# Optimization experiments

Measured on AMD Instinct MI355X. Metric: run time of the kernel, lower is better.

The kernel has to match this reference:

```python
import jax, jax.numpy as jnp
import numpy as np

B, N, K = 8, 2048, 20  # clouds, points per cloud, kNN neighbors
NUM_CLASSES = 40


def _mlp3(x, w1, b1, w2, b2, w3, b3):
    x = jax.nn.relu(x @ w1 + b1)
    x = jax.nn.relu(x @ w2 + b2)
    return jax.nn.relu(x @ w3 + b3)


def _dynamic_edge_conv(x, w1, b1, w2, b2, w3, b3):
    # x: [B, N, D]. Recompute kNN graph in feature space (per cloud),
    # build edge features [x_i, x_j - x_i], MLP, max-aggregate over neighbors.
    s = jnp.sum(x * x, axis=-1)  # [B, N]
    d2 = s[:, :, None] + s[:, None, :] - 2.0 * jnp.einsum('bnd,bmd->bnm', x, x)  # [B,N,N]
    _, idx = jax.lax.top_k(-d2, K)  # [B, N, K], includes self (dist 0), matching torch_cluster.knn(x, x)
    xj = jax.vmap(lambda xb, ib: xb[ib])(x, idx)  # gather neighbors [B, N, K, D]
    xi = jnp.broadcast_to(x[:, :, None, :], xj.shape)
    e = jnp.concatenate([xi, xj - xi], axis=-1)  # [B, N, K, 2D]
    h = _mlp3(e, w1, b1, w2, b2, w3, b3)  # [B, N, K, H]
    return jnp.max(h, axis=2)  # max aggregation -> [B, N, H]


def setup_inputs() -> dict:
    key = jax.random.key(0)
    ks = jax.random.split(key, 32)

    def w(k, shape):
        fan_in = shape[0]
        return (jax.random.normal(k, shape, dtype=jnp.float32) / np.sqrt(fan_in)).astype(jnp.float32)

    inp = {
        'pos': jax.random.normal(ks[0], (B * N, 3), dtype=jnp.float32),
        'batch': jnp.repeat(jnp.arange(B, dtype=jnp.int64), N),
        # conv1 MLP: 6 -> 64 -> 64 -> 64
        'c1w1': w(ks[1], (6, 64)),   'c1b1': jnp.zeros((64,), jnp.float32),
        'c1w2': w(ks[2], (64, 64)),  'c1b2': jnp.zeros((64,), jnp.float32),
        'c1w3': w(ks[3], (64, 64)),  'c1b3': jnp.zeros((64,), jnp.float32),
        # conv2 MLP: 128 -> 128 -> 128 -> 256
        'c2w1': w(ks[4], (128, 128)), 'c2b1': jnp.zeros((128,), jnp.float32),
        'c2w2': w(ks[5], (128, 128)), 'c2b2': jnp.zeros((128,), jnp.float32),
        'c2w3': w(ks[6], (128, 256)), 'c2b3': jnp.zeros((256,), jnp.float32),
        # classifier head
        'l0w': w(ks[7], (256, 512)),  'l0b': jnp.zeros((512,), jnp.float32),
        'l1w': w(ks[8], (512, 256)),  'l1b': jnp.zeros((256,), jnp.float32),
        'l2w': w(ks[9], (256, 256)),  'l2b': jnp.zeros((256,), jnp.float32),
        'l3w': w(ks[10], (256, NUM_CLASSES)), 'l3b': jnp.zeros((NUM_CLASSES,), jnp.float32),
    }
    return inp


def reference(pos, batch,
              c1w1, c1b1, c1w2, c1b2, c1w3, c1b3,
              c2w1, c2b1, c2w2, c2b2, c2w3, c2b3,
              l0w, l0b, l1w, l1b, l2w, l2b, l3w, l3b):
    # batch is a contiguous equal-size partition: reshape to [B, N, 3]
    x = pos.reshape(B, N, 3)
    x = _dynamic_edge_conv(x, c1w1, c1b1, c1w2, c1b2, c1w3, c1b3)   # [B, N, 64]
    x = _dynamic_edge_conv(x, c2w1, c2b1, c2w2, c2b2, c2w3, c2b3)   # [B, N, 256]
    x = jax.nn.relu(x @ l0w + l0b)                                   # [B, N, 512]
    x = jnp.max(x, axis=1)                                           # global_max_pool -> [B, 512]
    x = jax.nn.relu(x @ l1w + l1b)
    x = jax.nn.relu(x @ l2w + l2b)
    # dropout(p=0.5) is identity at inference
    x = x @ l3w + l3b
    return jax.nn.log_softmax(x, axis=-1)  # [B, NUM_CLASSES]
```

## Files before the change

### kernel.cpp

```cpp
#include <hip/hip_runtime.h>
#include <hip/hip_bf16.h>
#include <math.h>

#define BB 8
#define NN 2048
#define KK 20

typedef short bf16x8 __attribute__((ext_vector_type(8)));
typedef float f32x4 __attribute__((ext_vector_type(4)));

__device__ __forceinline__ unsigned short f2bf(float f) {
  unsigned u = __float_as_uint(f);
  u += 0x7FFFu + ((u >> 16) & 1u);
  return (unsigned short)(u >> 16);
}
__device__ __forceinline__ float bf2f(unsigned short h) {
  return __uint_as_float(((unsigned)h) << 16);
}

__device__ __forceinline__ void topk_insert(float d, int m, float (&bd)[KK], int (&bi)[KK],
                                            float& worst, int& wslot) {
  if (d < worst) {
#pragma unroll
    for (int j = 0; j < KK; ++j) {
      if (j == wslot) { bd[j] = d; bi[j] = m; }
    }
    float w = -INFINITY;
    int s = 0;
#pragma unroll
    for (int j = 0; j < KK; ++j) {
      if (bd[j] > w) { w = bd[j]; s = j; }
    }
    worst = w;
    wslot = s;
  }
}

__device__ __forceinline__ void sins20(float (&s)[KK], float d) {
#pragma unroll
  for (int q = 0; q < KK - 1; ++q) s[q] = fminf(s[q], fmaxf(s[q + 1], d));
  s[KK - 1] = fminf(s[KK - 1], d);
}

__device__ __forceinline__ float knn1_dist(float sn, float ssq,
                                           float x0, float x1, float x2,
                                           float y0, float y1, float y2) {
  const float dot = fmaf(x0, y0, fmaf(x1, y1, x2 * y2));
  return fmaf(-2.f, dot, sn + ssq);
}

__global__ __launch_bounds__(256) void knn1_part(const float* __restrict__ pos,
                                                 float* __restrict__ candd,
                                                 int* __restrict__ candi) {
  __shared__ float xs0[256], xs1[256], xs2[256], ss[256];
  const int bid = blockIdx.x;
  const int b = bid >> 6;
  const int nc = (bid >> 3) & 7;
  const int mc = bid & 7;
  const int t = threadIdx.x;
  const float* posb = pos + (size_t)b * NN * 3;
  {
    const int m = mc * 256 + t;
    const float a0 = posb[m * 3 + 0];
    const float a1 = posb[m * 3 + 1];
    const float a2 = posb[m * 3 + 2];
    xs0[t] = a0; xs1[t] = a1; xs2[t] = a2;
    ss[t] = a0 * a0 + a1 * a1 + a2 * a2;
  }
  __syncthreads();
  const int n = nc * 256 + t;
  const float xn0 = posb[n * 3 + 0];
  const float xn1 = posb[n * 3 + 1];
  const float xn2 = posb[n * 3 + 2];
  const float sn = xn0 * xn0 + xn1 * xn1 + xn2 * xn2;

  float s[KK];
#pragma unroll
  for (int q = 0; q < KK; ++q) s[q] = INFINITY;
  for (int lm = 0; lm < 256; lm += 8) {
    float dv[8];
#pragma unroll
    for (int u = 0; u < 8; ++u)
      dv[u] = knn1_dist(sn, ss[lm + u], xn0, xn1, xn2, xs0[lm + u], xs1[lm + u], xs2[lm + u]);
#pragma unroll
    for (int u = 0; u < 8; ++u) sins20(s, dv[u]);
  }
  const float tau = s[0];

  int cA = 0;
  for (int lm = 0; lm < 256; lm += 8) {
#pragma unroll
    for (int u = 0; u < 8; ++u) {
      const float d = knn1_dist(sn, ss[lm + u], xn0, xn1, xn2, xs0[lm + u], xs1[lm + u], xs2[lm + u]);
      cA += (d < tau) ? 1 : 0;
    }
  }

  int posA = 0, posB = cA;
  const int rbase = mc * 256;
  const size_t obase = ((size_t)(b * 8 + mc) * KK) * 2048 + n;
  for (int lm = 0; lm < 256; lm += 8) {
#pragma unroll
    for (int u = 0; u < 8; ++u) {
      const float d = knn1_dist(sn, ss[lm + u], xn0, xn1, xn2, xs0[lm + u], xs1[lm + u], xs2[lm + u]);
      if (d < tau) {
        candd[obase + (size_t)posA * 2048] = d;
        candi[obase + (size_t)posA * 2048] = rbase + lm + u;
        ++posA;
      } else if (d == tau && posB < KK) {
        candd[obase + (size_t)posB * 2048] = d;
        candi[obase + (size_t)posB * 2048] = rbase + lm + u;
        ++posB;
      }
    }
  }
}

template <int NCH, int G>
__global__ __launch_bounds__(256) void merge_topk2(const float* __restrict__ candd,
                                                   const int* __restrict__ candi,
                                                   int* __restrict__ idx_out) {
  const int gid = blockIdx.x * 256 + threadIdx.x;
  const int pt = gid / G;
  const int sub = gid % G;
  const int b = pt >> 11, n = pt & 2047;
  constexpr int CPT = NCH / G;
  float bd[KK]; int bi[KK];
#pragma unroll
  for (int j = 0; j < KK; ++j) { bd[j] = INFINITY; bi[j] = 0; }
  float worst = INFINITY;
  int wslot = 0;
#pragma unroll
  for (int cc = 0; cc < CPT; ++cc) {
    const int c = sub * CPT + cc;
    const size_t base = ((size_t)(b * NCH + c) * KK) * 2048 + n;
    float dv[KK]; int iv[KK];
#pragma unroll
    for (int j = 0; j < KK; ++j) dv[j] = candd[base + (size_t)j * 2048];
#pragma unroll
    for (int j = 0; j < KK; ++j) iv[j] = candi[base + (size_t)j * 2048];
#pragma unroll
    for (int j = 0; j < KK; ++j) topk_insert(dv[j], iv[j], bd, bi, worst, wslot);
  }
#pragma unroll
  for (int stride = 1; stride < G; stride <<= 1) {
    float od[KK]; int oi[KK];
#pragma unroll
    for (int q = 0; q < KK; ++q) {
      od[q] = __shfl_xor(bd[q], stride);
      oi[q] = __shfl_xor(bi[q], stride);
    }
#pragma unroll
    for (int q = 0; q < KK; ++q) topk_insert(od[q], oi[q], bd, bi, worst, wslot);
  }
  if (sub == 0) {
    int* op = idx_out + (size_t)pt * KK;
#pragma unroll
    for (int j = 0; j < KK; ++j) op[j] = bi[j];
  }
}

__global__ __launch_bounds__(256) void pre1_kernel(const float* __restrict__ pos,
                                                   const float* __restrict__ w1,
                                                   const float* __restrict__ b1,
                                                   float* __restrict__ U1,
                                                   float* __restrict__ V1) {
  const int t = threadIdx.x;
  const int c = t & 63;
  const int n = blockIdx.x * 4 + (t >> 6);
  const float p0 = pos[(size_t)n * 3 + 0];
  const float p1 = pos[(size_t)n * 3 + 1];
  const float p2 = pos[(size_t)n * 3 + 2];
  const float wt0 = w1[0 * 64 + c], wt1 = w1[1 * 64 + c], wt2 = w1[2 * 64 + c];
  const float wb0 = w1[3 * 64 + c], wb1 = w1[4 * 64 + c], wb2 = w1[5 * 64 + c];
  float v = p0 * wb0 + p1 * wb1 + p2 * wb2;
  float u = p0 * (wt0 - wb0) + p1 * (wt1 - wb1) + p2 * (wt2 - wb2) + b1[c];
  U1[(size_t)n * 64 + c] = u;
  V1[(size_t)n * 64 + c] = v;
}

__global__ __launch_bounds__(256) void pre2_kernel(const float* __restrict__ x1,
                                                   const float* __restrict__ w1,
                                                   const float* __restrict__ b1,
                                                   float* __restrict__ U,
                                                   float* __restrict__ V) {
  __shared__ float X[64][68];
  const int nbase = blockIdx.x * 64;
  const int t = threadIdx.x;
  for (int it = t; it < 1024; it += 256) {
    const int r = it >> 4, q = it & 15;
    *(float4*)&X[r][q * 4] = *(const float4*)&x1[(size_t)(nbase + r) * 64 + q * 4];
  }
  __syncthreads();
  const int ty = t >> 4, tx = t & 15;
  const int c0 = tx * 8;
  float accT[4][8], accB[4][8];
#pragma unroll
  for (int u = 0; u < 4; ++u)
#pragma unroll
    for (int i = 0; i < 8; ++i) { accT[u][i] = 0.f; accB[u][i] = 0.f; }
  for (int d0 = 0; d0 < 64; d0 += 4) {
    float4 a[4];
#pragma unroll
    for (int u = 0; u < 4; ++u) a[u] = *(const float4*)&X[ty * 4 + u][d0];
#pragma unroll
    for (int dd = 0; dd < 4; ++dd) {
      const float4 t0 = *(const float4*)&w1[(size_t)(d0 + dd) * 128 + c0];
      const float4 t1 = *(const float4*)&w1[(size_t)(d0 + dd) * 128 + c0 + 4];
      const float4 bb0 = *(const float4*)&w1[(size_t)(64 + d0 + dd) * 128 + c0];
      const float4 bb1 = *(const float4*)&w1[(size_t)(64 + d0 + dd) * 128 + c0 + 4];
#pragma unroll
      for (int u = 0; u < 4; ++u) {
        const float av = (dd == 0) ? a[u].x : (dd == 1) ? a[u].y : (dd == 2) ? a[u].z : a[u].w;
        accT[u][0] = fmaf(av, t0.x, accT[u][0]);
        accT[u][1] = fmaf(av, t0.y, accT[u][1]);
        accT[u][2] = fmaf(av, t0.z, accT[u][2]);
        accT[u][3] = fmaf(av, t0.w, accT[u][3]);
        accT[u][4] = fmaf(av, t1.x, accT[u][4]);
        accT[u][5] = fmaf(av, t1.y, accT[u][5]);
        accT[u][6] = fmaf(av, t1.z, accT[u][6]);
        accT[u][7] = fmaf(av, t1.w, accT[u][7]);
        accB[u][0] = fmaf(av, bb0.x, accB[u][0]);
        accB[u][1] = fmaf(av, bb0.y, accB[u][1]);
        accB[u][2] = fmaf(av, bb0.z, accB[u][2]);
        accB[u][3] = fmaf(av, bb0.w, accB[u][3]);
        accB[u][4] = fmaf(av, bb1.x, accB[u][4]);
        accB[u][5] = fmaf(av, bb1.y, accB[u][5]);
        accB[u][6] = fmaf(av, bb1.z, accB[u][6]);
        accB[u][7] = fmaf(av, bb1.w, accB[u][7]);
      }
    }
  }
  const float4 bA = *(const float4*)&b1[c0];
  const float4 bB = *(const float4*)&b1[c0 + 4];
#pragma unroll
  for (int u = 0; u < 4; ++u) {
    const size_t row = (size_t)(nbase + ty * 4 + u) * 128 + c0;
    float4 u0, u1, v0, v1;
    v0 = make_float4(accB[u][0], accB[u][1], accB[u][2], accB[u][3]);
    v1 = make_float4(accB[u][4], accB[u][5], accB[u][6], accB[u][7]);
    u0.x = accT[u][0] - accB[u][0] + bA.x;
    u0.y = accT[u][1] - accB[u][1] + bA.y;
    u0.z = accT[u][2] - accB[u][2] + bA.z;
    u0.w = accT[u][3] - accB[u][3] + bA.w;
    u1.x = accT[u][4] - accB[u][4] + bB.x;
    u1.y = accT[u][5] - accB[u][5] + bB.y;
    u1.z = accT[u][6] - accB[u][6] + bB.z;
    u1.w = accT[u][7] - accB[u][7] + bB.w;
    *(float4*)&U[row] = u0;
    *(float4*)&U[row + 4] = u1;
    *(float4*)&V[row] = v0;
    *(float4*)&V[row + 4] = v1;
  }
}

__global__ __launch_bounds__(256) void wprep_kernel(
    const float* __restrict__ c2w2, const float* __restrict__ c2w3,
    const float* __restrict__ c1w2, const float* __restrict__ c1w3,
    const float* __restrict__ l0w,
    unsigned short* __restrict__ w2t, unsigned short* __restrict__ w3t,
    unsigned short* __restrict__ c1w2hi, unsigned short* __restrict__ c1w2lo,
    unsigned short* __restrict__ c1w3hi, unsigned short* __restrict__ c1w3lo,
    unsigned short* __restrict__ l0thi, unsigned short* __restrict__ l0tlo) {
  const int i = blockIdx.x * 256 + threadIdx.x;
  if (i < 16384) {
    const int d = i >> 7, c = i & 127;
    w2t[c * 128 + d] = f2bf(c2w2[i]);
  } else if (i < 49152) {
    const int j = i - 16384;
    const int d = j >> 8, c = j & 255;
    w3t[c * 128 + d] = f2bf(c2w3[j]);
  } else if (i < 53248) {
    const int j = i - 49152;
    const int d = j >> 6, c = j & 63;
    const float v = c1w2[j];
    const unsigned short h = f2bf(v);
    c1w2hi[c * 64 + d] = h;
    c1w2lo[c * 64 + d] = f2bf(v - bf2f(h));
  } else if (i < 57344) {
    const int j = i - 53248;
    const int d = j >> 6, c = j & 63;
    const float v = c1w3[j];
    const unsigned short h = f2bf(v);
    c1w3hi[c * 64 + d] = h;
    c1w3lo[c * 64 + d] = f2bf(v - bf2f(h));
  } else if (i < 188416) {
    const int j = i - 57344;
    const int d = j >> 9, c = j & 511;
    const float v = l0w[j];
    const unsigned short h = f2bf(v);
    l0thi[c * 256 + d] = h;
    l0tlo[c * 256 + d] = f2bf(v - bf2f(h));
  }
}

__global__ __launch_bounds__(256) void conv1_kernel(
    const float* __restrict__ U1, const float* __restrict__ V1,
    const int* __restrict__ idx,
    const unsigned short* __restrict__ w2hi, const unsigned short* __restrict__ w2lo,
    const float* __restrict__ b2,
    const unsigned short* __restrict__ w3hi, const unsigned short* __restrict__ w3lo,
    const float* __restrict__ b3,
    float* __restrict__ xout) {
  __shared__ __align__(16) unsigned short A[160][2][76];
  __shared__ unsigned int pm[8][64];
  const int bid = blockIdx.x;
  const int b = bid >> 8;
  const int pbase = (bid & 255) * 8;
  const int t = threadIdx.x;
  const int wave = t >> 6, lane = t & 63;
  const int lrow = lane & 15;
  const int lk8 = (lane >> 4) * 8;
  const int c = wave * 16 + lrow;

  for (int it = t; it < 2560; it += 256) {
    const int r = it >> 4, q = it & 15;
    const int p = r / 20, k = r - (r / 20) * 20;
    const int n = b * NN + pbase + p;
    const int j = b * NN + idx[(size_t)n * KK + k];
    const float4 uv = *(const float4*)&U1[(size_t)n * 64 + q * 4];
    const float4 vv = *(const float4*)&V1[(size_t)j * 64 + q * 4];
    float e[4];
    e[0] = fmaxf(uv.x + vv.x, 0.f);
    e[1] = fmaxf(uv.y + vv.y, 0.f);
    e[2] = fmaxf(uv.z + vv.z, 0.f);
    e[3] = fmaxf(uv.w + vv.w, 0.f);
    ushort4 hi, lo;
    hi.x = f2bf(e[0]); lo.x = f2bf(e[0] - bf2f(hi.x));
    hi.y = f2bf(e[1]); lo.y = f2bf(e[1] - bf2f(hi.y));
    hi.z = f2bf(e[2]); lo.z = f2bf(e[2] - bf2f(hi.z));
    hi.w = f2bf(e[3]); lo.w = f2bf(e[3] - bf2f(hi.w));
    *(ushort4*)&A[r][0][q * 4] = hi;
    *(ushort4*)&A[r][1][q * 4] = lo;
  }
  for (int i = t; i < 512; i += 256) ((unsigned int*)pm)[i] = 0u;
  __syncthreads();

  {
    bf16x8 whi[2], wlo[2];
#pragma unroll
    for (int ks = 0; ks < 2; ++ks) {
      whi[ks] = *(const bf16x8*)&w2hi[(size_t)c * 64 + ks * 32 + lk8];
      wlo[ks] = *(const bf16x8*)&w2lo[(size_t)c * 64 + ks * 32 + lk8];
    }
    f32x4 acc2[10];
#pragma unroll
    for (int mt = 0; mt < 10; ++mt) {
      bf16x8 ahi[2], alo[2];
#pragma unroll
      for (int ks = 0; ks < 2; ++ks) {
        ahi[ks] = *(const bf16x8*)&A[mt * 16 + lrow][0][ks * 32 + lk8];
        alo[ks] = *(const bf16x8*)&A[mt * 16 + lrow][1][ks * 32 + lk8];
      }
      f32x4 acc = {0.f, 0.f, 0.f, 0.f};
#pragma unroll
      for (int ks = 0; ks < 2; ++ks) {
        acc = __builtin_amdgcn_mfma_f32_16x16x32_bf16(ahi[ks], whi[ks], acc, 0, 0, 0);
        acc = __builtin_amdgcn_mfma_f32_16x16x32_bf16(ahi[ks], wlo[ks], acc, 0, 0, 0);
        acc = __builtin_amdgcn_mfma_f32_16x16x32_bf16(alo[ks], whi[ks], acc, 0, 0, 0);
      }
      acc2[mt] = acc;
    }
    __syncthreads();
    const float bias = b2[c];
#pragma unroll
    for (int mt = 0; mt < 10; ++mt) {
      const int r0 = mt * 16 + ((lane >> 4) << 2);
#pragma unroll
      for (int reg = 0; reg < 4; ++reg) {
        const float v = fmaxf(acc2[mt][reg] + bias, 0.f);
        const unsigned short h = f2bf(v);
        A[r0 + reg][0][c] = h;
        A[r0 + reg][1][c] = f2bf(v - bf2f(h));
      }
    }
  }
  __syncthreads();

  {
    bf16x8 whi[2], wlo[2];
#pragma unroll
    for (int ks = 0; ks < 2; ++ks) {
      whi[ks] = *(const bf16x8*)&w3hi[(size_t)c * 64 + ks * 32 + lk8];
      wlo[ks] = *(const bf16x8*)&w3lo[(size_t)c * 64 + ks * 32 + lk8];
    }
    const float bias = b3[c];
#pragma unroll
    for (int mt = 0; mt < 10; ++mt) {
      bf16x8 ahi[2], alo[2];
#pragma unroll
      for (int ks = 0; ks < 2; ++ks) {
        ahi[ks] = *(const bf16x8*)&A[mt * 16 + lrow][0][ks * 32 + lk8];
        alo[ks] = *(const bf16x8*)&A[mt * 16 + lrow][1][ks * 32 + lk8];
      }
      f32x4 acc = {0.f, 0.f, 0.f, 0.f};
#pragma unroll
      for (int ks = 0; ks < 2; ++ks) {
        acc = __builtin_amdgcn_mfma_f32_16x16x32_bf16(ahi[ks], whi[ks], acc, 0, 0, 0);
        acc = __builtin_amdgcn_mfma_f32_16x16x32_bf16(ahi[ks], wlo[ks], acc, 0, 0, 0);
        acc = __builtin_amdgcn_mfma_f32_16x16x32_bf16(alo[ks], whi[ks], acc, 0, 0, 0);
      }
      const int r0 = mt * 16 + ((lane >> 4) << 2);
      const float v0 = fmaxf(acc[0] + bias, 0.f);
      const float v1 = fmaxf(acc[1] + bias, 0.f);
      const float v2 = fmaxf(acc[2] + bias, 0.f);
      const float v3 = fmaxf(acc[3] + bias, 0.f);
      if (r0 / 20 == (r0 + 3) / 20) {
        atomicMax(&pm[r0 / 20][c], __float_as_uint(fmaxf(fmaxf(v0, v1), fmaxf(v2, v3))));
      } else {
        atomicMax(&pm[(r0 + 0) / 20][c], __float_as_uint(v0));
        atomicMax(&pm[(r0 + 1) / 20][c], __float_as_uint(v1));
        atomicMax(&pm[(r0 + 2) / 20][c], __float_as_uint(v2));
        atomicMax(&pm[(r0 + 3) / 20][c], __float_as_uint(v3));
      }
    }
  }
  __syncthreads();

  {
    const int p = t >> 5;
    const int cc = (t & 31) * 2;
    float2 o;
    o.x = __uint_as_float(pm[p][cc]);
    o.y = __uint_as_float(pm[p][cc + 1]);
    *(float2*)&xout[((size_t)(b * NN + pbase + p)) * 64 + cc] = o;
  }
}

__global__ __launch_bounds__(256) void xsplit_kernel(const float* __restrict__ x1,
                                                     unsigned short* __restrict__ xhi,
                                                     unsigned short* __restrict__ xlo,
                                                     float* __restrict__ s) {
  const int e = blockIdx.x * 256 + threadIdx.x;
  const int n = e >> 3, q = e & 7;
  const float4 v0 = *(const float4*)&x1[(size_t)n * 64 + q * 8];
  const float4 v1 = *(const float4*)&x1[(size_t)n * 64 + q * 8 + 4];
  float ps = v0.x * v0.x + v0.y * v0.y + v0.z * v0.z + v0.w * v0.w +
             v1.x * v1.x + v1.y * v1.y + v1.z * v1.z + v1.w * v1.w;
  ps += __shfl_xor(ps, 1);
  ps += __shfl_xor(ps, 2);
  ps += __shfl_xor(ps, 4);
  if (q == 0) s[n] = ps;
  const float vv[8] = {v0.x, v0.y, v0.z, v0.w, v1.x, v1.y, v1.z, v1.w};
  unsigned short hb[8], lb[8];
#pragma unroll
  for (int i = 0; i < 8; ++i) {
    hb[i] = f2bf(vv[i]);
    lb[i] = f2bf(vv[i] - bf2f(hb[i]));
  }
  *(ushort4*)&xhi[(size_t)n * 64 + q * 8] = make_ushort4(hb[0], hb[1], hb[2], hb[3]);
  *(ushort4*)&xhi[(size_t)n * 64 + q * 8 + 4] = make_ushort4(hb[4], hb[5], hb[6], hb[7]);
  *(ushort4*)&xlo[(size_t)n * 64 + q * 8] = make_ushort4(lb[0], lb[1], lb[2], lb[3]);
  *(ushort4*)&xlo[(size_t)n * 64 + q * 8 + 4] = make_ushort4(lb[4], lb[5], lb[6], lb[7]);
}

__global__ __launch_bounds__(256) void d2sel_kernel(const unsigned short* __restrict__ xhi,
                                                    const unsigned short* __restrict__ xlo,
                                                    const float* __restrict__ s,
                                                    float* __restrict__ candd,
                                                    int* __restrict__ candi) {
  __shared__ __align__(16) unsigned short SBUF[4 * 128 * 72];
  __shared__ float sA[128], sB[128];
  float (*Tt)[132] = (float(*)[132])SBUF;
  const int bid = blockIdx.x;
  const int b = bid >> 8;
  const int tile = bid & 255;
  const int ti = tile >> 4, tj = tile & 15;
  const int i0 = ti * 128, j0 = tj * 128;
  const int gb = b * NN;
  const int t = threadIdx.x;
  const int wave = t >> 6, lane = t & 63;
  const int lrow = lane & 15;
  const int lk8 = (lane >> 4) * 8;

  for (int it = t; it < 4096; it += 256) {
    const int part = it >> 10;
    const int r = (it >> 3) & 127;
    const int g = it & 7;
    const unsigned short* src = (part == 0) ? xhi : (part == 1) ? xlo
                               : (part == 2) ? xhi : xlo;
    const int base = (part < 2) ? i0 : j0;
    *(uint4*)&SBUF[part * 9216 + r * 72 + g * 8] =
        *(const uint4*)&src[((size_t)(gb + base + r)) * 64 + g * 8];
  }
  if (t < 128) sA[t] = s[gb + i0 + t];
  else sB[t - 128] = s[gb + j0 + (t - 128)];
  __syncthreads();

  bf16x8 ahi[2][2], alo[2][2];
#pragma unroll
  for (int mt = 0; mt < 2; ++mt) {
    const int r = wave * 32 + mt * 16 + lrow;
#pragma unroll
    for (int ks = 0; ks < 2; ++ks) {
      ahi[mt][ks] = *(const bf16x8*)&SBUF[0 * 9216 + r * 72 + ks * 32 + lk8];
      alo[mt][ks] = *(const bf16x8*)&SBUF[1 * 9216 + r * 72 + ks * 32 + lk8];
    }
  }
  f32x4 acc[2][8];
#pragma unroll
  for (int mt = 0; mt < 2; ++mt)
#pragma unroll
    for (int nt = 0; nt < 8; ++nt) acc[mt][nt] = (f32x4){0.f, 0.f, 0.f, 0.f};
#pragma unroll
  for (int nt = 0; nt < 8; ++nt) {
    bf16x8 bhi[2], blo[2];
#pragma unroll
    for (int ks = 0; ks < 2; ++ks) {
      bhi[ks] = *(const bf16x8*)&SBUF[2 * 9216 + (nt * 16 + lrow) * 72 + ks * 32 + lk8];
      blo[ks] = *(const bf16x8*)&SBUF[3 * 9216 + (nt * 16 + lrow) * 72 + ks * 32 + lk8];
    }
#pragma unroll
    for (int mt = 0; mt < 2; ++mt) {
#pragma unroll
      for (int ks = 0; ks < 2; ++ks) {
        acc[mt][nt] = __builtin_amdgcn_mfma_f32_16x16x32_bf16(ahi[mt][ks], bhi[ks], acc[mt][nt], 0, 0, 0);
        acc[mt][nt] = __builtin_amdgcn_mfma_f32_16x16x32_bf16(ahi[mt][ks], blo[ks], acc[mt][nt], 0, 0, 0);
        acc[mt][nt] = __builtin_amdgcn_mfma_f32_16x16x32_bf16(alo[mt][ks], bhi[ks], acc[mt][nt], 0, 0, 0);
      }
    }
  }
  __syncthreads();

#pragma unroll
  for (int mt = 0; mt < 2; ++mt) {
    const int ib = wave * 32 + mt * 16 + ((lane >> 4) << 2);
#pragma unroll
    for (int nt = 0; nt < 8; ++nt) {
      const int jj = nt * 16 + lrow;
      const float sj = sB[jj];
      float4 o;
      o.x = sA[ib + 0] + sj - 2.f * acc[mt][nt][0];
      o.y = sA[ib + 1] + sj - 2.f * acc[mt][nt][1];
      o.z = sA[ib + 2] + sj - 2.f * acc[mt][nt][2];
      o.w = sA[ib + 3] + sj - 2.f * acc[mt][nt][3];
      *(float4*)&Tt[jj][ib] = o;
    }
  }
  __syncthreads();

  const int j = t >> 1, h = t & 1;
  float sl[KK];
#pragma unroll
  for (int q = 0; q < KK; ++q) sl[q] = INFINITY;
  for (int r4 = 0; r4 < 16; ++r4) {
    const float4 v = *(const float4*)&Tt[j][h * 64 + r4 * 4];
    sins20(sl, v.x);
    sins20(sl, v.y);
    sins20(sl, v.z);
    sins20(sl, v.w);
  }
  {
    float od[KK];
#pragma unroll
    for (int q = 0; q < KK; ++q) od[q] = __shfl_xor(sl[q], 1);
#pragma unroll
    for (int q = 0; q < KK; ++q) sins20(sl, od[q]);
  }
  const float tau = sl[0];

  int cA = 0, cB = 0;
  for (int r4 = 0; r4 < 16; ++r4) {
    const float4 v = *(const float4*)&Tt[j][h * 64 + r4 * 4];
    cA += (v.x < tau) + (v.y < tau) + (v.z < tau) + (v.w < tau);
    cB += (v.x == tau) + (v.y == tau) + (v.z == tau) + (v.w == tau);
  }
  const int pA = __shfl_xor(cA, 1);
  const int pB = __shfl_xor(cB, 1);
  const int nA = cA + pA;
  int posA = h ? pA : 0;
  int posB = nA + (h ? pB : 0);

  const size_t obase = ((size_t)(b * 16 + ti) * KK) * 2048 + (j0 + j);
  for (int r4 = 0; r4 < 16; ++r4) {
    const float4 v = *(const float4*)&Tt[j][h * 64 + r4 * 4];
    const float dd[4] = {v.x, v.y, v.z, v.w};
#pragma unroll
    for (int u = 0; u < 4; ++u) {
      const float d = dd[u];
      const int row = i0 + h * 64 + r4 * 4 + u;
      if (d < tau) {
        candd[obase + (size_t)posA * 2048] = d;
        candi[obase + (size_t)posA * 2048] = row;
        ++posA;
      } else if (d == tau && posB < KK) {
        candd[obase + (size_t)posB * 2048] = d;
        candi[obase + (size_t)posB * 2048] = row;
        ++posB;
      }
    }
  }
}

__global__ __launch_bounds__(256) void conv2_kernel(
    const float* __restrict__ U, const float* __restrict__ V,
    const int* __restrict__ idx,
    const unsigned short* __restrict__ w2t, const float* __restrict__ b2,
    const unsigned short* __restrict__ w3t, const float* __restrict__ b3,
    unsigned short* __restrict__ x2hi, unsigned short* __restrict__ x2lo) {
  __shared__ __align__(16) unsigned short E[80][136];
  __shared__ unsigned int pm[4][256];
  const int bid = blockIdx.x;
  const int b = bid >> 9;
  const int pbase = (bid & 511) * 4;
  const int t = threadIdx.x;
  const int wave = t >> 6, lane = t & 63;
  const int lrow = lane & 15;
  const int lk8 = (lane >> 4) * 8;

  for (int it = t; it < 2560; it += 256) {
    const int r = it >> 5, q = it & 31;
    const int p = r / 20, k = r - (r / 20) * 20;
    const int n = b * NN + pbase + p;
    const int j = b * NN + idx[(size_t)n * KK + k];
    const float4 uv = *(const float4*)&U[(size_t)n * 128 + q * 4];
    const float4 vv = *(const float4*)&V[(size_t)j * 128 + q * 4];
    ushort4 h;
    h.x = f2bf(fmaxf(uv.x + vv.x, 0.f));
    h.y = f2bf(fmaxf(uv.y + vv.y, 0.f));
    h.z = f2bf(fmaxf(uv.z + vv.z, 0.f));
    h.w = f2bf(fmaxf(uv.w + vv.w, 0.f));
    *(ushort4*)&E[r][q * 4] = h;
  }
  for (int i = t; i < 1024; i += 256) ((unsigned int*)pm)[i] = 0u;
  __syncthreads();

  {
    bf16x8 wf[2][4];
#pragma unroll
    for (int nt2 = 0; nt2 < 2; ++nt2) {
      const int ntg = wave * 2 + nt2;
#pragma unroll
      for (int ks = 0; ks < 4; ++ks)
        wf[nt2][ks] = *(const bf16x8*)&w2t[(size_t)(ntg * 16 + lrow) * 128 + ks * 32 + lk8];
    }
    f32x4 a0buf[5], a1buf[5];
#pragma unroll
    for (int mt = 0; mt < 5; ++mt) {
      bf16x8 af[4];
#pragma unroll
      for (int ks = 0; ks < 4; ++ks)
        af[ks] = *(const bf16x8*)&E[mt * 16 + lrow][ks * 32 + lk8];
      f32x4 acc0 = {0.f, 0.f, 0.f, 0.f};
      f32x4 acc1 = {0.f, 0.f, 0.f, 0.f};
#pragma unroll
      for (int ks = 0; ks < 4; ++ks) {
        acc0 = __builtin_amdgcn_mfma_f32_16x16x32_bf16(af[ks], wf[0][ks], acc0, 0, 0, 0);
        acc1 = __builtin_amdgcn_mfma_f32_16x16x32_bf16(af[ks], wf[1][ks], acc1, 0, 0, 0);
      }
      a0buf[mt] = acc0;
      a1buf[mt] = acc1;
    }
    __syncthreads();
    const float bias0 = b2[wave * 32 + lrow];
    const float bias1 = b2[wave * 32 + 16 + lrow];
#pragma unroll
    for (int mt = 0; mt < 5; ++mt) {
      const int r0 = mt * 16 + ((lane >> 4) << 2);
      const int c0 = wave * 32 + lrow;
#pragma unroll
      for (int reg = 0; reg < 4; ++reg) {
        E[r0 + reg][c0]      = f2bf(fmaxf(a0buf[mt][reg] + bias0, 0.f));
        E[r0 + reg][c0 + 16] = f2bf(fmaxf(a1buf[mt][reg] + bias1, 0.f));
      }
    }
  }
  __syncthreads();

  {
    bf16x8 wf[4][4];
#pragma unroll
    for (int nt4 = 0; nt4 < 4; ++nt4) {
      const int ntg = wave * 4 + nt4;
#pragma unroll
      for (int ks = 0; ks < 4; ++ks)
        wf[nt4][ks] = *(const bf16x8*)&w3t[(size_t)(ntg * 16 + lrow) * 128 + ks * 32 + lk8];
    }
#pragma unroll
    for (int mt = 0; mt < 5; ++mt) {
      bf16x8 af[4];
#pragma unroll
      for (int ks = 0; ks < 4; ++ks)
        af[ks] = *(const bf16x8*)&E[mt * 16 + lrow][ks * 32 + lk8];
      f32x4 acc[4];
#pragma unroll
      for (int nt4 = 0; nt4 < 4; ++nt4) acc[nt4] = (f32x4){0.f, 0.f, 0.f, 0.f};
#pragma unroll
      for (int ks = 0; ks < 4; ++ks) {
#pragma unroll
        for (int nt4 = 0; nt4 < 4; ++nt4)
          acc[nt4] = __builtin_amdgcn_mfma_f32_16x16x32_bf16(af[ks], wf[nt4][ks], acc[nt4], 0, 0, 0);
      }
      const int r0 = mt * 16 + ((lane >> 4) << 2);
      const int pa = r0 / 20;
      const int pb = (r0 + 3) / 20;
#pragma unroll
      for (int nt4 = 0; nt4 < 4; ++nt4) {
        const int c = wave * 64 + nt4 * 16 + lrow;
        const float bias = b3[c];
        float v0 = fmaxf(acc[nt4][0] + bias, 0.f);
        float v1 = fmaxf(acc[nt4][1] + bias, 0.f);
        float v2 = fmaxf(acc[nt4][2] + bias, 0.f);
        float v3 = fmaxf(acc[nt4][3] + bias, 0.f);
        if (pa == pb) {
          atomicMax(&pm[pa][c], __float_as_uint(fmaxf(fmaxf(v0, v1), fmaxf(v2, v3))));
        } else {
          atomicMax(&pm[(r0 + 0) / 20][c], __float_as_uint(v0));
          atomicMax(&pm[(r0 + 1) / 20][c], __float_as_uint(v1));
          atomicMax(&pm[(r0 + 2) / 20][c], __float_as_uint(v2));
          atomicMax(&pm[(r0 + 3) / 20][c], __float_as_uint(v3));
        }
      }
    }
  }
  __syncthreads();

  {
    const int p = t >> 6;
    const int c0 = (t & 63) * 4;
    const float4 o = *(const float4*)&pm[p][c0];
    ushort4 hi, lo;
    hi.x = f2bf(o.x); lo.x = f2bf(o.x - bf2f(hi.x));
    hi.y = f2bf(o.y); lo.y = f2bf(o.y - bf2f(hi.y));
    hi.z = f2bf(o.z); lo.z = f2bf(o.z - bf2f(hi.z));
    hi.w = f2bf(o.w); lo.w = f2bf(o.w - bf2f(hi.w));
    const size_t base = ((size_t)b * NN + pbase + p) * 256 + c0;
    *(ushort4*)&x2hi[base] = hi;
    *(ushort4*)&x2lo[base] = lo;
  }
}

__global__ __launch_bounds__(256) void l0_kernel(
    const unsigned short* __restrict__ x2hi, const unsigned short* __restrict__ x2lo,
    const unsigned short* __restrict__ l0thi, const unsigned short* __restrict__ l0tlo,
    const float* __restrict__ bias, float* __restrict__ gp) {
  __shared__ __align__(16) unsigned short Ahi[64][72];
  __shared__ __align__(16) unsigned short Alo[64][72];
  __shared__ unsigned int pm[256];
  const int bid = blockIdx.x;
  const int cblk = bid & 1;
  const int mblk = (bid >> 1) & 31;
  const int b = bid >> 6;
  const int t = threadIdx.x;
  const int wave = t >> 6, lane = t & 63;
  const int lrow = lane & 15;
  const int lk8 = (lane >> 4) * 8;
  const size_t rowbase = (size_t)(b * NN + mblk * 64);
  const int cbase = cblk * 256;

  pm[t] = 0u;

  f32x4 acc[4][4];
#pragma unroll
  for (int mt = 0; mt < 4; ++mt)
#pragma unroll
    for (int nt = 0; nt < 4; ++nt) acc[mt][nt] = (f32x4){0.f, 0.f, 0.f, 0.f};

  for (int kc = 0; kc < 4; ++kc) {
    for (int it = t; it < 1024; it += 256) {
      const int buf = it >> 9;
      const int r = (it >> 3) & 63;
      const int g = it & 7;
      const unsigned short* src = buf ? x2lo : x2hi;
      const uint4 v = *(const uint4*)&src[(rowbase + r) * 256 + kc * 64 + g * 8];
      if (buf) *(uint4*)&Alo[r][g * 8] = v;
      else     *(uint4*)&Ahi[r][g * 8] = v;
    }
    __syncthreads();

    bf16x8 bhi[4][2], blo[4][2];
#pragma unroll
    for (int nt = 0; nt < 4; ++nt) {
      const size_t c = (size_t)(cbase + wave * 64 + nt * 16 + lrow);
#pragma unroll
      for (int ks = 0; ks < 2; ++ks) {
        bhi[nt][ks] = *(const bf16x8*)&l0thi[c * 256 + kc * 64 + ks * 32 + lk8];
        blo[nt][ks] = *(const bf16x8*)&l0tlo[c * 256 + kc * 64 + ks * 32 + lk8];
      }
    }
#pragma unroll
    for (int mt = 0; mt < 4; ++mt) {
      bf16x8 ahi[2], alo[2];
#pragma unroll
      for (int ks = 0; ks < 2; ++ks) {
        ahi[ks] = *(const bf16x8*)&Ahi[mt * 16 + lrow][ks * 32 + lk8];
        alo[ks] = *(const bf16x8*)&Alo[mt * 16 + lrow][ks * 32 + lk8];
      }
#pragma unroll
      for (int nt = 0; nt < 4; ++nt) {
#pragma unroll
        for (int ks = 0; ks < 2; ++ks) {
          acc[mt][nt] = __builtin_amdgcn_mfma_f32_16x16x32_bf16(ahi[ks], bhi[nt][ks], acc[mt][nt], 0, 0, 0);
          acc[mt][nt] = __builtin_amdgcn_mfma_f32_16x16x32_bf16(ahi[ks], blo[nt][ks], acc[mt][nt], 0, 0, 0);
          acc[mt][nt] = __builtin_amdgcn_mfma_f32_16x16x32_bf16(alo[ks], bhi[nt][ks], acc[mt][nt], 0, 0, 0);
        }
      }
    }
    __syncthreads();
  }

#pragma unroll
  for (int nt = 0; nt < 4; ++nt) {
    const int cl = wave * 64 + nt * 16 + lrow;
    const float bv = bias[cbase + cl];
    float mx = 0.f;
#pragma unroll
    for (int mt = 0; mt < 4; ++mt)
#pragma unroll
      for (int reg = 0; reg < 4; ++reg)
        mx = fmaxf(mx, fmaxf(acc[mt][nt][reg] + bv, 0.f));
    atomicMax(&pm[cl], __float_as_uint(mx));
  }
  __syncthreads();
  gp[((size_t)(b * 32 + mblk)) * 512 + cbase + t] = __uint_as_float(pm[t]);
}

__global__ __launch_bounds__(256) void head_kernel(
    const float* __restrict__ gp,
    const float* __restrict__ l1w, const float* __restrict__ l1b,
    const float* __restrict__ l2w, const float* __restrict__ l2b,
    const float* __restrict__ l3w, const float* __restrict__ l3b,
    float* __restrict__ out) {
  __shared__ float g[512];
  __shared__ float h1[256];
  __shared__ float h2[256];
  __shared__ float logits[40];
  __shared__ float lse_s;
  const int b = blockIdx.x;
  const int t = threadIdx.x;
  for (int cidx = t; cidx < 512; cidx += 256) {
    float m = gp[(size_t)(b * 32) * 512 + cidx];
    for (int ch = 1; ch < 32; ++ch) m = fmaxf(m, gp[(size_t)(b * 32 + ch) * 512 + cidx]);
    g[cidx] = m;
  }
  __syncthreads();
  {
    float acc = 0.f;
    for (int d = 0; d < 512; d += 4) {
      const float4 gv = *(const float4*)&g[d];
      acc = fmaf(gv.x, l1w[(size_t)d * 256 + t], acc);
      acc = fmaf(gv.y, l1w[(size_t)(d + 1) * 256 + t], acc);
      acc = fmaf(gv.z, l1w[(size_t)(d + 2) * 256 + t], acc);
      acc = fmaf(gv.w, l1w[(size_t)(d + 3) * 256 + t], acc);
    }
    h1[t] = fmaxf(acc + l1b[t], 0.f);
  }
  __syncthreads();
  {
    float acc = 0.f;
    for (int d = 0; d < 256; d += 4) {
      const float4 hv = *(const float4*)&h1[d];
      acc = fmaf(hv.x, l2w[(size_t)d * 256 + t], acc);
      acc = fmaf(hv.y, l2w[(size_t)(d + 1) * 256 + t], acc);
      acc = fmaf(hv.z, l2w[(size_t)(d + 2) * 256 + t], acc);
      acc = fmaf(hv.w, l2w[(size_t)(d + 3) * 256 + t], acc);
    }
    h2[t] = fmaxf(acc + l2b[t], 0.f);
  }
  __syncthreads();
  if (t < 40) {
    float acc = 0.f;
    for (int d = 0; d < 256; ++d) acc = fmaf(h2[d], l3w[(size_t)d * 40 + t], acc);
    logits[t] = acc + l3b[t];
  }
  __syncthreads();
  if (t == 0) {
    float M = -INFINITY;
    for (int j = 0; j < 40; ++j) M = fmaxf(M, logits[j]);
    float ssum = 0.f;
    for (int j = 0; j < 40; ++j) ssum += expf(logits[j] - M);
    lse_s = M + logf(ssum);
  }
  __syncthreads();
  if (t < 40) out[(size_t)b * 40 + t] = logits[t] - lse_s;
}

extern "C" void kernel_launch(void* const* d_in, const int* in_sizes, int n_in,
                              void* d_out, int out_size, void* d_ws, size_t ws_size,
                              hipStream_t stream) {
  const float* pos  = (const float*)d_in[0];
  const float* c1w1 = (const float*)d_in[2];
  const float* c1b1 = (const float*)d_in[3];
  const float* c1w2 = (const float*)d_in[4];
  const float* c1b2 = (const float*)d_in[5];
  const float* c1w3 = (const float*)d_in[6];
  const float* c1b3 = (const float*)d_in[7];
  const float* c2w1 = (const float*)d_in[8];
  const float* c2b1 = (const float*)d_in[9];
  const float* c2w2 = (const float*)d_in[10];
  const float* c2b2 = (const float*)d_in[11];
  const float* c2w3 = (const float*)d_in[12];
  const float* c2b3 = (const float*)d_in[13];
  const float* l0w  = (const float*)d_in[14];
  const float* l0b  = (const float*)d_in[15];
  const float* l1w  = (const float*)d_in[16];
  const float* l1b  = (const float*)d_in[17];
  const float* l2w  = (const float*)d_in[18];
  const float* l2b  = (const float*)d_in[19];
  const float* l3w  = (const float*)d_in[20];
  const float* l3b  = (const float*)d_in[21];
  float* out = (float*)d_out;

  char* ws = (char*)d_ws;
  float* x1    = (float*)(ws + 0);
  int*   idx1  = (int*)  (ws + ((size_t)20 << 20));
  int*   idx2  = (int*)  (ws + ((size_t)22 << 20));
  float* gp    = (float*)(ws + ((size_t)24 << 20));
  unsigned short* w2t    = (unsigned short*)(ws + ((size_t)24 << 20) + (512 << 10));
  unsigned short* w3t    = (unsigned short*)(ws + ((size_t)24 << 20) + (544 << 10));
  unsigned short* c1w2hi = (unsigned short*)(ws + ((size_t)24 << 20) + (608 << 10));
  unsigned short* c1w2lo = (unsigned short*)(ws + ((size_t)24 << 20) + (616 << 10));
  unsigned short* c1w3hi = (unsigned short*)(ws + ((size_t)24 << 20) + (624 << 10));
  unsigned short* c1w3lo = (unsigned short*)(ws + ((size_t)24 << 20) + (632 << 10));
  float* candd = (float*)(ws + ((size_t)25 << 20));
  int*   candi = (int*)  (ws + ((size_t)46 << 20));
  float* U1 = (float*)(ws + ((size_t)25 << 20));
  float* V1 = (float*)(ws + ((size_t)29 << 20));
  float* U  = (float*)(ws + ((size_t)46 << 20));
  float* Vv = (float*)(ws + ((size_t)54 << 20));
  unsigned short* xhi  = (unsigned short*)(ws + ((size_t)68 << 20));
  unsigned short* xlo  = (unsigned short*)(ws + ((size_t)70 << 20));
  float*          sbuf = (float*)         (ws + ((size_t)72 << 20));
  unsigned short* x2hi = (unsigned short*)(ws + ((size_t)73 << 20));
  unsigned short* x2lo = (unsigned short*)(ws + ((size_t)81 << 20));
  unsigned short* l0thi = (unsigned short*)(ws + ((size_t)89 << 20));
  unsigned short* l0tlo = (unsigned short*)(ws + ((size_t)89 << 20) + (256 << 10));

  wprep_kernel<<<736, 256, 0, stream>>>(c2w2, c2w3, c1w2, c1w3, l0w,
                                        w2t, w3t, c1w2hi, c1w2lo, c1w3hi, c1w3lo,
                                        l0thi, l0tlo);
  knn1_part<<<512, 256, 0, stream>>>(pos, candd, candi);
  merge_topk2<8, 4><<<256, 256, 0, stream>>>(candd, candi, idx1);
  pre1_kernel<<<4096, 256, 0, stream>>>(pos, c1w1, c1b1, U1, V1);
  conv1_kernel<<<2048, 256, 0, stream>>>(U1, V1, idx1, c1w2hi, c1w2lo, c1b2,
                                         c1w3hi, c1w3lo, c1b3, x1);
  xsplit_kernel<<<512, 256, 0, stream>>>(x1, xhi, xlo, sbuf);
  d2sel_kernel<<<2048, 256, 0, stream>>>(xhi, xlo, sbuf, candd, candi);
  merge_topk2<16, 8><<<512, 256, 0, stream>>>(candd, candi, idx2);
  pre2_kernel<<<256, 256, 0, stream>>>(x1, c2w1, c2b1, U, Vv);
  conv2_kernel<<<4096, 256, 0, stream>>>(U, Vv, idx2, w2t, c2b2, w3t, c2b3, x2hi, x2lo);
  l0_kernel<<<512, 256, 0, stream>>>(x2hi, x2lo, l0thi, l0tlo, l0b, gp);
  head_kernel<<<8, 256, 0, stream>>>(gp, l1w, l1b, l2w, l2b, l3w, l3b, out);
}
```

Before: 492.5 us.

## Use 512 threads in d2sel kernel, splitting top-k selection four ways

```diff
diff --git a/kernel.cpp b/kernel.cpp
--- a/kernel.cpp
+++ b/kernel.cpp
@@ -454,7 +454,7 @@
   *(ushort4*)&xlo[(size_t)n * 64 + q * 8 + 4] = make_ushort4(lb[4], lb[5], lb[6], lb[7]);
 }
 
-__global__ __launch_bounds__(256) void d2sel_kernel(const unsigned short* __restrict__ xhi,
+__global__ __launch_bounds__(512) void d2sel_kernel(const unsigned short* __restrict__ xhi,
                                                     const unsigned short* __restrict__ xlo,
                                                     const float* __restrict__ s,
                                                     float* __restrict__ candd,
@@ -473,7 +473,7 @@
   const int lrow = lane & 15;
   const int lk8 = (lane >> 4) * 8;
 
-  for (int it = t; it < 4096; it += 256) {
+  for (int it = t; it < 4096; it += 512) {
     const int part = it >> 10;
     const int r = (it >> 3) & 127;
     const int g = it & 7;
@@ -484,24 +484,21 @@
         *(const uint4*)&src[((size_t)(gb + base + r)) * 64 + g * 8];
   }
   if (t < 128) sA[t] = s[gb + i0 + t];
-  else sB[t - 128] = s[gb + j0 + (t - 128)];
-  __syncthreads();
-
-  bf16x8 ahi[2][2], alo[2][2];
-#pragma unroll
-  for (int mt = 0; mt < 2; ++mt) {
-    const int r = wave * 32 + mt * 16 + lrow;
+  else if (t < 256) sB[t - 128] = s[gb + j0 + (t - 128)];
+  __syncthreads();
+
+  bf16x8 ahi[2], alo[2];
+  {
+    const int r = wave * 16 + lrow;
 #pragma unroll
     for (int ks = 0; ks < 2; ++ks) {
-      ahi[mt][ks] = *(const bf16x8*)&SBUF[0 * 9216 + r * 72 + ks * 32 + lk8];
-      alo[mt][ks] = *(const bf16x8*)&SBUF[1 * 9216 + r * 72 + ks * 32 + lk8];
-    }
-  }
-  f32x4 acc[2][8];
-#pragma unroll
-  for (int mt = 0; mt < 2; ++mt)
-#pragma unroll
-    for (int nt = 0; nt < 8; ++nt) acc[mt][nt] = (f32x4){0.f, 0.f, 0.f, 0.f};
+      ahi[ks] = *(const bf16x8*)&SBUF[0 * 9216 + r * 72 + ks * 32 + lk8];
+      alo[ks] = *(const bf16x8*)&SBUF[1 * 9216 + r * 72 + ks * 32 + lk8];
+    }
+  }
+  f32x4 acc[8];
+#pragma unroll
+  for (int nt = 0; nt < 8; ++nt) acc[nt] = (f32x4){0.f, 0.f, 0.f, 0.f};
 #pragma unroll
   for (int nt = 0; nt < 8; ++nt) {
     bf16x8 bhi[2], blo[2];
@@ -511,40 +508,36 @@
       blo[ks] = *(const bf16x8*)&SBUF[3 * 9216 + (nt * 16 + lrow) * 72 + ks * 32 + lk8];
     }
 #pragma unroll
-    for (int mt = 0; mt < 2; ++mt) {
-#pragma unroll
-      for (int ks = 0; ks < 2; ++ks) {
-        acc[mt][nt] = __builtin_amdgcn_mfma_f32_16x16x32_bf16(ahi[mt][ks], bhi[ks], acc[mt][nt], 0, 0, 0);
-        acc[mt][nt] = __builtin_amdgcn_mfma_f32_16x16x32_bf16(ahi[mt][ks], blo[ks], acc[mt][nt], 0, 0, 0);
-        acc[mt][nt] = __builtin_amdgcn_mfma_f32_16x16x32_bf16(alo[mt][ks], bhi[ks], acc[mt][nt], 0, 0, 0);
-      }
-    }
-  }
-  __syncthreads();
-
-#pragma unroll
-  for (int mt = 0; mt < 2; ++mt) {
-    const int ib = wave * 32 + mt * 16 + ((lane >> 4) << 2);
+    for (int ks = 0; ks < 2; ++ks) {
+      acc[nt] = __builtin_amdgcn_mfma_f32_16x16x32_bf16(ahi[ks], bhi[ks], acc[nt], 0, 0, 0);
+      acc[nt] = __builtin_amdgcn_mfma_f32_16x16x32_bf16(ahi[ks], blo[ks], acc[nt], 0, 0, 0);
+      acc[nt] = __builtin_amdgcn_mfma_f32_16x16x32_bf16(alo[ks], bhi[ks], acc[nt], 0, 0, 0);
+    }
+  }
+  __syncthreads();
+
+  {
+    const int ib = wave * 16 + ((lane >> 4) << 2);
 #pragma unroll
     for (int nt = 0; nt < 8; ++nt) {
       const int jj = nt * 16 + lrow;
       const float sj = sB[jj];
       float4 o;
-      o.x = sA[ib + 0] + sj - 2.f * acc[mt][nt][0];
-      o.y = sA[ib + 1] + sj - 2.f * acc[mt][nt][1];
-      o.z = sA[ib + 2] + sj - 2.f * acc[mt][nt][2];
-      o.w = sA[ib + 3] + sj - 2.f * acc[mt][nt][3];
+      o.x = sA[ib + 0] + sj - 2.f * acc[nt][0];
+      o.y = sA[ib + 1] + sj - 2.f * acc[nt][1];
+      o.z = sA[ib + 2] + sj - 2.f * acc[nt][2];
+      o.w = sA[ib + 3] + sj - 2.f * acc[nt][3];
       *(float4*)&Tt[jj][ib] = o;
     }
   }
   __syncthreads();
 
-  const int j = t >> 1, h = t & 1;
+  const int j = t >> 2, h = t & 3;
   float sl[KK];
 #pragma unroll
   for (int q = 0; q < KK; ++q) sl[q] = INFINITY;
-  for (int r4 = 0; r4 < 16; ++r4) {
-    const float4 v = *(const float4*)&Tt[j][h * 64 + r4 * 4];
+  for (int r4 = 0; r4 < 8; ++r4) {
+    const float4 v = *(const float4*)&Tt[j][h * 32 + r4 * 4];
     sins20(sl, v.x);
     sins20(sl, v.y);
     sins20(sl, v.z);
@@ -556,29 +549,42 @@
     for (int q = 0; q < KK; ++q) od[q] = __shfl_xor(sl[q], 1);
 #pragma unroll
     for (int q = 0; q < KK; ++q) sins20(sl, od[q]);
+#pragma unroll
+    for (int q = 0; q < KK; ++q) od[q] = __shfl_xor(sl[q], 2);
+#pragma unroll
+    for (int q = 0; q < KK; ++q) sins20(sl, od[q]);
   }
   const float tau = sl[0];
 
   int cA = 0, cB = 0;
-  for (int r4 = 0; r4 < 16; ++r4) {
-    const float4 v = *(const float4*)&Tt[j][h * 64 + r4 * 4];
+  for (int r4 = 0; r4 < 8; ++r4) {
+    const float4 v = *(const float4*)&Tt[j][h * 32 + r4 * 4];
     cA += (v.x < tau) + (v.y < tau) + (v.z < tau) + (v.w < tau);
     cB += (v.x == tau) + (v.y == tau) + (v.z == tau) + (v.w == tau);
   }
-  const int pA = __shfl_xor(cA, 1);
-  const int pB = __shfl_xor(cB, 1);
-  const int nA = cA + pA;
-  int posA = h ? pA : 0;
-  int posB = nA + (h ? pB : 0);
+  const int lb = lane & ~3;
+  int aArr[4], bArr[4];
+#pragma unroll
+  for (int g = 0; g < 4; ++g) {
+    aArr[g] = __shfl(cA, lb + g);
+    bArr[g] = __shfl(cB, lb + g);
+  }
+  const int nAtot = aArr[0] + aArr[1] + aArr[2] + aArr[3];
+  int prefA = 0, prefB = 0;
+  if (h > 0) { prefA += aArr[0]; prefB += bArr[0]; }
+  if (h > 1) { prefA += aArr[1]; prefB += bArr[1]; }
+  if (h > 2) { prefA += aArr[2]; prefB += bArr[2]; }
+  int posA = prefA;
+  int posB = nAtot + prefB;
 
   const size_t obase = ((size_t)(b * 16 + ti) * KK) * 2048 + (j0 + j);
-  for (int r4 = 0; r4 < 16; ++r4) {
-    const float4 v = *(const float4*)&Tt[j][h * 64 + r4 * 4];
+  for (int r4 = 0; r4 < 8; ++r4) {
+    const float4 v = *(const float4*)&Tt[j][h * 32 + r4 * 4];
     const float dd[4] = {v.x, v.y, v.z, v.w};
 #pragma unroll
     for (int u = 0; u < 4; ++u) {
       const float d = dd[u];
-      const int row = i0 + h * 64 + r4 * 4 + u;
+      const int row = i0 + h * 32 + r4 * 4 + u;
       if (d < tau) {
         candd[obase + (size_t)posA * 2048] = d;
         candi[obase + (size_t)posA * 2048] = row;
@@ -935,7 +941,7 @@
   conv1_kernel<<<2048, 256, 0, stream>>>(U1, V1, idx1, c1w2hi, c1w2lo, c1b2,
                                          c1w3hi, c1w3lo, c1b3, x1);
   xsplit_kernel<<<512, 256, 0, stream>>>(x1, xhi, xlo, sbuf);
-  d2sel_kernel<<<2048, 256, 0, stream>>>(xhi, xlo, sbuf, candd, candi);
+  d2sel_kernel<<<2048, 512, 0, stream>>>(xhi, xlo, sbuf, candd, candi);
   merge_topk2<16, 8><<<512, 256, 0, stream>>>(candd, candi, idx2);
   pre2_kernel<<<256, 256, 0, stream>>>(x1, c2w1, c2b1, U, Vv);
   conv2_kernel<<<4096, 256, 0, stream>>>(U, Vv, idx2, w2t, c2b2, w3t, c2b3, x2hi, x2lo);
```

After: 511.4 us. +3.8%, slower.
